# Performance work log

Hardware: AMD Instinct MI355X
Metric: run time of the kernel (lower is better)

Reference implementation:

```python
import jax, jax.numpy as jnp
import numpy as np

TOP_K = 2
EPS = 1e-8

def setup_inputs() -> dict:
    key = jax.random.key(0)
    k1, k2 = jax.random.split(key)
    T, D, E = 16384, 4096, 128  # tokens, d_model, num_experts
    x = jax.random.normal(k1, (T, D), dtype=jnp.float32)
    W = jax.random.normal(k2, (E, D), dtype=jnp.float32) * (1.0 / np.sqrt(D))
    b = jnp.zeros((E,), dtype=jnp.float32)
    return {"x": x, "W": W, "b": b}

def reference(x, W, b):
    # gate linear: [T, D] @ [D, E] -> [T, E]
    logits = jnp.einsum('td,ed->te', x, W) + b
    probs = jax.nn.softmax(logits, axis=-1)
    top_k_probs, top_k_indices = jax.lax.top_k(probs, TOP_K)
    top_k_probs = top_k_probs / (jnp.sum(top_k_probs, axis=-1, keepdims=True) + EPS)
    return (top_k_indices, top_k_probs)
```

## Files before the change

### kernel.cpp

```cpp
#include <hip/hip_runtime.h>
#include <math.h>


#define T_TOKENS 16384
#define D_K      4096
#define N_EXP    128
#define TOK_BLK  64
#define KSTEP    64
#define NITER    (D_K / KSTEP)

typedef float  f32x4  __attribute__((ext_vector_type(4)));
typedef short  bf16x8 __attribute__((ext_vector_type(8)));
typedef float  fragc  __attribute__((ext_vector_type(4)));

__device__ __forceinline__ unsigned short bf16_rne(float f) {
    unsigned u = __float_as_uint(f);
    u += 0x7FFFu + ((u >> 16) & 1u);
    return (unsigned short)(u >> 16);
}
__device__ __forceinline__ float bf16f(unsigned short h) {
    return __uint_as_float(((unsigned)h) << 16);
}

__device__ __forceinline__ int a_off(int G, int l) {
    const int L  = G * 64 + l;
    const int sw = ((L >> 3) ^ G) & 7;
    return (L << 4) ^ (sw << 4);
}

__global__ __launch_bounds__(256)
void prep_w(const float* __restrict__ W,
            short* __restrict__ wh, short* __restrict__ wl) {
    const int gid = blockIdx.x * 256 + threadIdx.x;
    const int l   = gid & 63;
    const int ntk = gid >> 6;
    const int e   = ((ntk & 7) << 4) + (l & 15);
    const int k   = ((ntk >> 3) << 5) + ((l >> 4) << 3);
    const float* src = W + (size_t)e * D_K + k;
    const f32x4 v0 = *(const f32x4*)src;
    const f32x4 v1 = *(const f32x4*)(src + 4);
    bf16x8 hv, lv;
#pragma unroll
    for (int j = 0; j < 8; ++j) {
        const float f = (j < 4) ? v0[j] : v1[j - 4];
        const unsigned short hh = bf16_rne(f);
        hv[j] = (short)hh;
        lv[j] = (short)bf16_rne(f - bf16f(hh));
    }
    *(bf16x8*)(wh + (size_t)gid * 8) = hv;
    *(bf16x8*)(wl + (size_t)gid * 8) = lv;
}

#define LOGSTRIDE 140
#define MERGE_OFF (64 * LOGSTRIDE * 4)
#define SMEM_SZ   (MERGE_OFF + 64 * 8 * 9 * 4)

__global__ __launch_bounds__(512, 2)
void router_mfma(const float* __restrict__ x,
                 const short* __restrict__ wh,
                 const short* __restrict__ wl,
                 const float* __restrict__ bvec,
                 float* __restrict__ out) {
    __shared__ __align__(16) char smem[SMEM_SZ];

    const int tid  = threadIdx.x;
    const int lane = tid & 63;
    const int w    = tid >> 6;
    const int wm   = w >> 2;
    const int wn   = w & 3;
    const int g    = blockIdx.x;

    const int s_tok = tid >> 3;
    const int s_kc8 = tid & 7;
    const float* xsrc = x + (size_t)(g * TOK_BLK + s_tok) * D_K + s_kc8 * 8;
    const int G_s   = ((s_kc8 >> 2) << 2) + (s_tok >> 4);
    const int l_s   = (s_tok & 15) | ((s_kc8 & 3) << 4);
    const int off_s = a_off(G_s, l_s);

    f32x4 ld0, ld1;
    auto issue = [&](int t) {
        const float* p = xsrc + (size_t)t * KSTEP;
        ld0 = *(const f32x4*)p;
        ld1 = *(const f32x4*)(p + 4);
    };
    auto commit = [&](int bufbase) {
        bf16x8 hv, lv;
#pragma unroll
        for (int j = 0; j < 8; ++j) {
            const float f = (j < 4) ? ld0[j] : ld1[j - 4];
            const unsigned short hh = bf16_rne(f);
            hv[j] = (short)hh;
            lv[j] = (short)bf16_rne(f - bf16f(hh));
        }
        *(bf16x8*)(smem + bufbase + off_s)        = hv;
        *(bf16x8*)(smem + bufbase + 8192 + off_s) = lv;
    };

    const short* base_h = wh + ((size_t)(wn * 2) * 64 + lane) * 8;
    const short* base_l = wl + ((size_t)(wn * 2) * 64 + lane) * 8;

    fragc acc[2][2];
#pragma unroll
    for (int mi = 0; mi < 2; ++mi)
#pragma unroll
        for (int nt = 0; nt < 2; ++nt)
            acc[mi][nt] = (fragc){0.f, 0.f, 0.f, 0.f};

    issue(0);
    commit(0);
    issue(1);
    __syncthreads();

    for (int t = 0; t < NITER; ++t) {
        const int cur = (t & 1) << 14;

        if (t + 1 < NITER) {
            commit(cur ^ (1 << 14));
            if (t + 2 < NITER) issue(t + 2);
        }

        bf16x8 bh[2][2], bl[2][2];
#pragma unroll
        for (int kb = 0; kb < 2; ++kb) {
            const size_t kofs = (size_t)(2 * t + kb) * 4096;
#pragma unroll
            for (int nt = 0; nt < 2; ++nt) {
                bh[kb][nt] = *(const bf16x8*)(base_h + kofs + nt * 512);
                bl[kb][nt] = *(const bf16x8*)(base_l + kofs + nt * 512);
            }
        }

#pragma unroll
        for (int kb = 0; kb < 2; ++kb) {
            bf16x8 ah[2], al[2];
#pragma unroll
            for (int mi = 0; mi < 2; ++mi) {
                const int off = a_off(kb * 4 + wm * 2 + mi, lane);
                ah[mi] = *(const bf16x8*)(smem + cur + off);
                al[mi] = *(const bf16x8*)(smem + cur + 8192 + off);
            }
#pragma unroll
            for (int mi = 0; mi < 2; ++mi)
#pragma unroll
                for (int nt = 0; nt < 2; ++nt) {
                    acc[mi][nt] = __builtin_amdgcn_mfma_f32_16x16x32_bf16(
                        ah[mi], bh[kb][nt], acc[mi][nt], 0, 0, 0);
                    acc[mi][nt] = __builtin_amdgcn_mfma_f32_16x16x32_bf16(
                        al[mi], bh[kb][nt], acc[mi][nt], 0, 0, 0);
                    acc[mi][nt] = __builtin_amdgcn_mfma_f32_16x16x32_bf16(
                        ah[mi], bl[kb][nt], acc[mi][nt], 0, 0, 0);
                }
        }
        __syncthreads();
    }

    float* lg = (float*)smem;
#pragma unroll
    for (int mi = 0; mi < 2; ++mi) {
        const int row0 = wm * 32 + mi * 16 + ((lane >> 4) << 2);
#pragma unroll
        for (int nt = 0; nt < 2; ++nt) {
            const int col = wn * 32 + nt * 16 + (lane & 15);
#pragma unroll
            for (int j = 0; j < 4; ++j)
                lg[(row0 + j) * LOGSTRIDE + col] = acc[mi][nt][j];
        }
    }
    __syncthreads();

    const int tok = tid & 63;
    const int q   = tid >> 6;
    const float* lrow = lg + tok * LOGSTRIDE + q * 16;
    const float* brow = bvec + q * 16;
    float v1 = -INFINITY, v2 = -INFINITY;
    int   i1 = 0, i2 = 0;
#pragma unroll
    for (int c = 0; c < 16; ++c) {
        const float lv = lrow[c] + brow[c];
        if (lv > v1)      { v2 = v1; i2 = i1; v1 = lv; i1 = c; }
        else if (lv > v2) { v2 = lv; i2 = c; }
    }
    float Z = 0.f;
#pragma unroll
    for (int c = 0; c < 16; ++c) Z += expf(lrow[c] + brow[c] - v1);

    float* mrow = (float*)(smem + MERGE_OFF) + (tok * 8 + q) * 9;
    mrow[0] = v1; mrow[1] = (float)(q * 16 + i1);
    mrow[2] = v2; mrow[3] = (float)(q * 16 + i2);
    mrow[4] = Z;
    __syncthreads();

    if (tid < 64) {
        const float* m0 = (float*)(smem + MERGE_OFF) + tid * 72;
        float V1 = m0[0], I1 = m0[1], V2 = m0[2], I2 = m0[3], Zs = m0[4];
#pragma unroll
        for (int q2 = 1; q2 < 8; ++q2) {
            const float* mq = m0 + q2 * 9;
            const float a1 = mq[0], ai1 = mq[1], a2 = mq[2], ai2 = mq[3], Zq = mq[4];
            const float M  = fmaxf(V1, a1);
            Zs = Zs * expf(V1 - M) + Zq * expf(a1 - M);
            if (a1 > V1)      { V2 = V1; I2 = I1; V1 = a1; I1 = ai1; }
            else if (a1 > V2) { V2 = a1; I2 = ai1; }
            if (a2 > V2)      { V2 = a2; I2 = ai2; }
        }
        const float p1 = 1.0f / Zs;
        const float p2 = expf(V2 - V1) / Zs;
        const float s  = p1 + p2 + 1e-8f;
        const int tokG = g * TOK_BLK + tid;
        float2* oidx  = (float2*)out;
        float2* oprob = ((float2*)out) + T_TOKENS;
        oidx[tokG]  = make_float2(I1, I2);
        oprob[tokG] = make_float2(p1 / s, p2 / s);
    }
}

extern "C" void kernel_launch(void* const* d_in, const int* in_sizes, int n_in,
                              void* d_out, int out_size, void* d_ws, size_t ws_size,
                              hipStream_t stream) {
    (void)in_sizes; (void)n_in; (void)out_size; (void)ws_size;
    const float* x = (const float*)d_in[0];
    const float* W = (const float*)d_in[1];
    const float* b = (const float*)d_in[2];
    float* out = (float*)d_out;
    short* wh = (short*)d_ws;
    short* wl = (short*)d_ws + (size_t)N_EXP * D_K;

    prep_w<<<dim3(256), dim3(256), 0, stream>>>(W, wh, wl);
    router_mfma<<<dim3(T_TOKENS / TOK_BLK), dim3(512), 0, stream>>>(x, wh, wl, b, out);
}
```

Measured before the change: 421.3 us.

## Load activations directly into registers and drop LDS staging and barriers

Each wave now loads its own x rows straight from global memory into registers, double-buffered two steps ahead. The bf16 hi/lo split is done in registers rather than written to LDS, which removes the per-iteration __syncthreads. The hi part is now a truncation instead of round-to-nearest, while the residual still carries the remainder. In exchange, each x element is loaded by the 4 waves that share the same wm rows, so global and L2 traffic for x goes up and register pressure rises.

```diff
diff --git a/kernel.cpp b/kernel.cpp
--- a/kernel.cpp
+++ b/kernel.cpp
@@ -6,8 +6,7 @@
 #define D_K      4096
 #define N_EXP    128
 #define TOK_BLK  64
-#define KSTEP    64
-#define NITER    (D_K / KSTEP)
+#define NITER    64
 
 typedef float  f32x4  __attribute__((ext_vector_type(4)));
 typedef short  bf16x8 __attribute__((ext_vector_type(8)));
@@ -20,12 +19,6 @@
 }
 __device__ __forceinline__ float bf16f(unsigned short h) {
     return __uint_as_float(((unsigned)h) << 16);
-}
-
-__device__ __forceinline__ int a_off(int G, int l) {
-    const int L  = G * 64 + l;
-    const int sw = ((L >> 3) ^ G) & 7;
-    return (L << 4) ^ (sw << 4);
 }
 
 __global__ __launch_bounds__(256)
@@ -70,31 +63,9 @@
     const int wn   = w & 3;
     const int g    = blockIdx.x;
 
-    const int s_tok = tid >> 3;
-    const int s_kc8 = tid & 7;
-    const float* xsrc = x + (size_t)(g * TOK_BLK + s_tok) * D_K + s_kc8 * 8;
-    const int G_s   = ((s_kc8 >> 2) << 2) + (s_tok >> 4);
-    const int l_s   = (s_tok & 15) | ((s_kc8 & 3) << 4);
-    const int off_s = a_off(G_s, l_s);
-
-    f32x4 ld0, ld1;
-    auto issue = [&](int t) {
-        const float* p = xsrc + (size_t)t * KSTEP;
-        ld0 = *(const f32x4*)p;
-        ld1 = *(const f32x4*)(p + 4);
-    };
-    auto commit = [&](int bufbase) {
-        bf16x8 hv, lv;
-#pragma unroll
-        for (int j = 0; j < 8; ++j) {
-            const float f = (j < 4) ? ld0[j] : ld1[j - 4];
-            const unsigned short hh = bf16_rne(f);
-            hv[j] = (short)hh;
-            lv[j] = (short)bf16_rne(f - bf16f(hh));
-        }
-        *(bf16x8*)(smem + bufbase + off_s)        = hv;
-        *(bf16x8*)(smem + bufbase + 8192 + off_s) = lv;
-    };
+    const float* arow0 = x + (size_t)(g * TOK_BLK + wm * 32 + (lane & 15)) * D_K
+                           + ((lane >> 4) << 3);
+    const float* arow1 = arow0 + (size_t)16 * D_K;
 
     const short* base_h = wh + ((size_t)(wn * 2) * 64 + lane) * 8;
     const short* base_l = wl + ((size_t)(wn * 2) * 64 + lane) * 8;
@@ -106,19 +77,22 @@
         for (int nt = 0; nt < 2; ++nt)
             acc[mi][nt] = (fragc){0.f, 0.f, 0.f, 0.f};
 
-    issue(0);
-    commit(0);
-    issue(1);
-    __syncthreads();
-
-    for (int t = 0; t < NITER; ++t) {
-        const int cur = (t & 1) << 14;
-
-        if (t + 1 < NITER) {
-            commit(cur ^ (1 << 14));
-            if (t + 2 < NITER) issue(t + 2);
-        }
-
+    f32x4 Aa[2][2][2], Ab[2][2][2];
+
+    auto loadA = [&](f32x4 (&A)[2][2][2], int t) {
+        const float* p0 = arow0 + (size_t)t * 64;
+        const float* p1 = arow1 + (size_t)t * 64;
+        A[0][0][0] = *(const f32x4*)(p0);
+        A[0][0][1] = *(const f32x4*)(p0 + 4);
+        A[0][1][0] = *(const f32x4*)(p0 + 32);
+        A[0][1][1] = *(const f32x4*)(p0 + 36);
+        A[1][0][0] = *(const f32x4*)(p1);
+        A[1][0][1] = *(const f32x4*)(p1 + 4);
+        A[1][1][0] = *(const f32x4*)(p1 + 32);
+        A[1][1][1] = *(const f32x4*)(p1 + 36);
+    };
+
+    auto step = [&](f32x4 (&A)[2][2][2], int t) {
         bf16x8 bh[2][2], bl[2][2];
 #pragma unroll
         for (int kb = 0; kb < 2; ++kb) {
@@ -129,29 +103,40 @@
                 bl[kb][nt] = *(const bf16x8*)(base_l + kofs + nt * 512);
             }
         }
-
-#pragma unroll
-        for (int kb = 0; kb < 2; ++kb) {
-            bf16x8 ah[2], al[2];
-#pragma unroll
-            for (int mi = 0; mi < 2; ++mi) {
-                const int off = a_off(kb * 4 + wm * 2 + mi, lane);
-                ah[mi] = *(const bf16x8*)(smem + cur + off);
-                al[mi] = *(const bf16x8*)(smem + cur + 8192 + off);
-            }
+        bf16x8 ah[2][2], al[2][2];
+#pragma unroll
+        for (int kb = 0; kb < 2; ++kb)
+#pragma unroll
+            for (int mi = 0; mi < 2; ++mi)
+#pragma unroll
+                for (int j = 0; j < 8; ++j) {
+                    const float f = (j < 4) ? A[mi][kb][0][j] : A[mi][kb][1][j - 4];
+                    const unsigned u  = __float_as_uint(f);
+                    const unsigned hu = u & 0xFFFF0000u;
+                    ah[kb][mi][j] = (short)(u >> 16);
+                    al[kb][mi][j] = (short)bf16_rne(f - __uint_as_float(hu));
+                }
+        if (t + 2 < NITER) loadA(A, t + 2);
+#pragma unroll
+        for (int kb = 0; kb < 2; ++kb)
 #pragma unroll
             for (int mi = 0; mi < 2; ++mi)
 #pragma unroll
                 for (int nt = 0; nt < 2; ++nt) {
                     acc[mi][nt] = __builtin_amdgcn_mfma_f32_16x16x32_bf16(
-                        ah[mi], bh[kb][nt], acc[mi][nt], 0, 0, 0);
+                        ah[kb][mi], bh[kb][nt], acc[mi][nt], 0, 0, 0);
                     acc[mi][nt] = __builtin_amdgcn_mfma_f32_16x16x32_bf16(
-                        al[mi], bh[kb][nt], acc[mi][nt], 0, 0, 0);
+                        al[kb][mi], bh[kb][nt], acc[mi][nt], 0, 0, 0);
                     acc[mi][nt] = __builtin_amdgcn_mfma_f32_16x16x32_bf16(
-                        ah[mi], bl[kb][nt], acc[mi][nt], 0, 0, 0);
+                        ah[kb][mi], bl[kb][nt], acc[mi][nt], 0, 0, 0);
                 }
-        }
-        __syncthreads();
+    };
+
+    loadA(Aa, 0);
+    loadA(Ab, 1);
+    for (int t = 0; t < NITER; t += 2) {
+        step(Aa, t);
+        step(Ab, t + 1);
     }
 
     float* lg = (float*)smem;
```

Result: slower. 457.3 us (+8.5%).

## Halve token tile to 32, give each wave one expert tile, raise occupancy

Applied to the files above, without the earlier changes.

Shrinks the per-block token tile from 64 to 32 so each of the 8 waves owns one 16-expert column tile and two 16-token row tiles. LDS per block drops and launch bounds request 4 blocks per CU instead of 2. The W fragment loads are issued before the x commit, and __syncthreads is replaced by an explicit lgkmcnt wait plus barrier. Each W fragment now feeds only 32 tokens instead of 64, so L2 traffic for W per token doubles in exchange for more blocks to hide latency.

```diff
diff --git a/kernel.cpp b/kernel.cpp
--- a/kernel.cpp
+++ b/kernel.cpp
@@ -5,13 +5,13 @@
 #define T_TOKENS 16384
 #define D_K      4096
 #define N_EXP    128
-#define TOK_BLK  64
-#define KSTEP    64
-#define NITER    (D_K / KSTEP)
+#define TOK_BLK  32
+#define NITER    64
 
 typedef float  f32x4  __attribute__((ext_vector_type(4)));
 typedef short  bf16x8 __attribute__((ext_vector_type(8)));
 typedef float  fragc  __attribute__((ext_vector_type(4)));
+typedef unsigned int u32;
 
 __device__ __forceinline__ unsigned short bf16_rne(float f) {
     unsigned u = __float_as_uint(f);
@@ -51,11 +51,11 @@
     *(bf16x8*)(wl + (size_t)gid * 8) = lv;
 }
 
-#define LOGSTRIDE 140
-#define MERGE_OFF (64 * LOGSTRIDE * 4)
-#define SMEM_SZ   (MERGE_OFF + 64 * 8 * 9 * 4)
-
-__global__ __launch_bounds__(512, 2)
+#define LOGSTRIDE 129
+#define MERGE_OFF (TOK_BLK * LOGSTRIDE * 4)
+#define SMEM_SZ   (MERGE_OFF + TOK_BLK * 8 * 9 * 4)
+
+__global__ __launch_bounds__(512, 4)
 void router_mfma(const float* __restrict__ x,
                  const short* __restrict__ wh,
                  const short* __restrict__ wl,
@@ -66,132 +66,137 @@
     const int tid  = threadIdx.x;
     const int lane = tid & 63;
     const int w    = tid >> 6;
-    const int wm   = w >> 2;
-    const int wn   = w & 3;
     const int g    = blockIdx.x;
 
-    const int s_tok = tid >> 3;
-    const int s_kc8 = tid & 7;
-    const float* xsrc = x + (size_t)(g * TOK_BLK + s_tok) * D_K + s_kc8 * 8;
-    const int G_s   = ((s_kc8 >> 2) << 2) + (s_tok >> 4);
-    const int l_s   = (s_tok & 15) | ((s_kc8 & 3) << 4);
-    const int off_s = a_off(G_s, l_s);
-
-    f32x4 ld0, ld1;
-    auto issue = [&](int t) {
-        const float* p = xsrc + (size_t)t * KSTEP;
-        ld0 = *(const f32x4*)p;
-        ld1 = *(const f32x4*)(p + 4);
+    const int s_tok = tid >> 4;
+    const int s_k4  = tid & 15;
+    const float* xsrc = x + (size_t)(g * TOK_BLK + s_tok) * D_K + s_k4 * 4;
+    const int kb_s  = s_k4 >> 3;
+    const int c_s   = s_k4 & 7;
+    const int mt_s  = s_tok >> 4;
+    const int l_s   = (s_tok & 15) | ((c_s >> 1) << 4);
+    const int off_s = a_off(kb_s * 2 + mt_s, l_s) + (c_s & 1) * 8;
+
+    f32x4 ld;
+    auto issue = [&](int t) { ld = *(const f32x4*)(xsrc + (size_t)t * 64); };
+    auto commit = [&](int bufbase) {
+        u32 h[2], lo[2];
+#pragma unroll
+        for (int p = 0; p < 2; ++p) {
+            u32 hw = 0, lw = 0;
+#pragma unroll
+            for (int j = 0; j < 2; ++j) {
+                const float f = ld[p * 2 + j];
+                const unsigned short hh = bf16_rne(f);
+                const unsigned short ll = bf16_rne(f - bf16f(hh));
+                hw |= (u32)hh << (16 * j);
+                lw |= (u32)ll << (16 * j);
+            }
+            h[p] = hw; lo[p] = lw;
+        }
+        *(uint2*)(smem + bufbase + off_s)        = make_uint2(h[0], h[1]);
+        *(uint2*)(smem + bufbase + 4096 + off_s) = make_uint2(lo[0], lo[1]);
     };
-    auto commit = [&](int bufbase) {
-        bf16x8 hv, lv;
-#pragma unroll
-        for (int j = 0; j < 8; ++j) {
-            const float f = (j < 4) ? ld0[j] : ld1[j - 4];
-            const unsigned short hh = bf16_rne(f);
-            hv[j] = (short)hh;
-            lv[j] = (short)bf16_rne(f - bf16f(hh));
-        }
-        *(bf16x8*)(smem + bufbase + off_s)        = hv;
-        *(bf16x8*)(smem + bufbase + 8192 + off_s) = lv;
-    };
-
-    const short* base_h = wh + ((size_t)(wn * 2) * 64 + lane) * 8;
-    const short* base_l = wl + ((size_t)(wn * 2) * 64 + lane) * 8;
-
-    fragc acc[2][2];
-#pragma unroll
-    for (int mi = 0; mi < 2; ++mi)
-#pragma unroll
-        for (int nt = 0; nt < 2; ++nt)
-            acc[mi][nt] = (fragc){0.f, 0.f, 0.f, 0.f};
+
+    const short* base_h = wh + ((size_t)w * 64 + lane) * 8;
+    const short* base_l = wl + ((size_t)w * 64 + lane) * 8;
+
+    fragc acc0 = (fragc){0.f, 0.f, 0.f, 0.f};
+    fragc acc1 = (fragc){0.f, 0.f, 0.f, 0.f};
 
     issue(0);
     commit(0);
     issue(1);
-    __syncthreads();
+    asm volatile("s_waitcnt lgkmcnt(0)\n\ts_barrier" ::: "memory");
 
     for (int t = 0; t < NITER; ++t) {
-        const int cur = (t & 1) << 14;
-
-        if (t + 1 < NITER) {
-            commit(cur ^ (1 << 14));
-            if (t + 2 < NITER) issue(t + 2);
-        }
-
-        bf16x8 bh[2][2], bl[2][2];
+        const int cur = (t & 1) << 13;
+
+        bf16x8 bh[2], bl[2];
 #pragma unroll
         for (int kb = 0; kb < 2; ++kb) {
             const size_t kofs = (size_t)(2 * t + kb) * 4096;
-#pragma unroll
-            for (int nt = 0; nt < 2; ++nt) {
-                bh[kb][nt] = *(const bf16x8*)(base_h + kofs + nt * 512);
-                bl[kb][nt] = *(const bf16x8*)(base_l + kofs + nt * 512);
+            bh[kb] = *(const bf16x8*)(base_h + kofs);
+            bl[kb] = *(const bf16x8*)(base_l + kofs);
+        }
+
+        if (t + 1 < NITER) {
+            commit(cur ^ 8192);
+            if (t + 2 < NITER) issue(t + 2);
+        }
+
+        bf16x8 ah[2][2], al[2][2];
+#pragma unroll
+        for (int kb = 0; kb < 2; ++kb)
+#pragma unroll
+            for (int mi = 0; mi < 2; ++mi) {
+                const int off = a_off(kb * 2 + mi, lane);
+                ah[kb][mi] = *(const bf16x8*)(smem + cur + off);
+                al[kb][mi] = *(const bf16x8*)(smem + cur + 4096 + off);
             }
-        }
 
 #pragma unroll
         for (int kb = 0; kb < 2; ++kb) {
-            bf16x8 ah[2], al[2];
-#pragma unroll
-            for (int mi = 0; mi < 2; ++mi) {
-                const int off = a_off(kb * 4 + wm * 2 + mi, lane);
-                ah[mi] = *(const bf16x8*)(smem + cur + off);
-                al[mi] = *(const bf16x8*)(smem + cur + 8192 + off);
+            acc0 = __builtin_amdgcn_mfma_f32_16x16x32_bf16(ah[kb][0], bh[kb], acc0, 0, 0, 0);
+            acc0 = __builtin_amdgcn_mfma_f32_16x16x32_bf16(al[kb][0], bh[kb], acc0, 0, 0, 0);
+            acc0 = __builtin_amdgcn_mfma_f32_16x16x32_bf16(ah[kb][0], bl[kb], acc0, 0, 0, 0);
+            acc1 = __builtin_amdgcn_mfma_f32_16x16x32_bf16(ah[kb][1], bh[kb], acc1, 0, 0, 0);
+            acc1 = __builtin_amdgcn_mfma_f32_16x16x32_bf16(al[kb][1], bh[kb], acc1, 0, 0, 0);
+            acc1 = __builtin_amdgcn_mfma_f32_16x16x32_bf16(ah[kb][1], bl[kb], acc1, 0, 0, 0);
+        }
+
+        asm volatile("s_waitcnt lgkmcnt(0)\n\ts_barrier" ::: "memory");
+    }
+    __syncthreads();
+
+    float* lg = (float*)smem;
+    {
+        const int col = w * 16 + (lane & 15);
+        const int r0  = (lane >> 4) << 2;
+#pragma unroll
+        for (int j = 0; j < 4; ++j) lg[(r0 + j) * LOGSTRIDE + col]      = acc0[j];
+#pragma unroll
+        for (int j = 0; j < 4; ++j) lg[(16 + r0 + j) * LOGSTRIDE + col] = acc1[j];
+    }
+    __syncthreads();
+
+    float* mg = (float*)(smem + MERGE_OFF);
+    if (tid < 256) {
+        const int tok = tid & 31;
+        const int q   = tid >> 5;
+        const float* lrow = lg + tok * LOGSTRIDE + q * 16;
+        f32x4 lv4[4], bv4[4];
+#pragma unroll
+        for (int i = 0; i < 4; ++i) lv4[i] = *(const f32x4*)(lrow + i * 4);
+#pragma unroll
+        for (int i = 0; i < 4; ++i) bv4[i] = *(const f32x4*)(bvec + q * 16 + i * 4);
+        float v1 = -INFINITY, v2 = -INFINITY;
+        int   i1 = 0, i2 = 0;
+#pragma unroll
+        for (int i = 0; i < 4; ++i)
+#pragma unroll
+            for (int j = 0; j < 4; ++j) {
+                const int   c  = i * 4 + j;
+                const float lv = lv4[i][j] + bv4[i][j];
+                if (lv > v1)      { v2 = v1; i2 = i1; v1 = lv; i1 = c; }
+                else if (lv > v2) { v2 = lv; i2 = c; }
             }
-#pragma unroll
-            for (int mi = 0; mi < 2; ++mi)
-#pragma unroll
-                for (int nt = 0; nt < 2; ++nt) {
-                    acc[mi][nt] = __builtin_amdgcn_mfma_f32_16x16x32_bf16(
-                        ah[mi], bh[kb][nt], acc[mi][nt], 0, 0, 0);
-                    acc[mi][nt] = __builtin_amdgcn_mfma_f32_16x16x32_bf16(
-                        al[mi], bh[kb][nt], acc[mi][nt], 0, 0, 0);
-                    acc[mi][nt] = __builtin_amdgcn_mfma_f32_16x16x32_bf16(
-                        ah[mi], bl[kb][nt], acc[mi][nt], 0, 0, 0);
-                }
-        }
-        __syncthreads();
-    }
-
-    float* lg = (float*)smem;
-#pragma unroll
-    for (int mi = 0; mi < 2; ++mi) {
-        const int row0 = wm * 32 + mi * 16 + ((lane >> 4) << 2);
-#pragma unroll
-        for (int nt = 0; nt < 2; ++nt) {
-            const int col = wn * 32 + nt * 16 + (lane & 15);
+        float Z = 0.f;
+#pragma unroll
+        for (int i = 0; i < 4; ++i)
 #pragma unroll
             for (int j = 0; j < 4; ++j)
-                lg[(row0 + j) * LOGSTRIDE + col] = acc[mi][nt][j];
-        }
+                Z += expf(lv4[i][j] + bv4[i][j] - v1);
+
+        float* mrow = mg + (tok * 8 + q) * 9;
+        mrow[0] = v1; mrow[1] = (float)(q * 16 + i1);
+        mrow[2] = v2; mrow[3] = (float)(q * 16 + i2);
+        mrow[4] = Z;
     }
     __syncthreads();
 
-    const int tok = tid & 63;
-    const int q   = tid >> 6;
-    const float* lrow = lg + tok * LOGSTRIDE + q * 16;
-    const float* brow = bvec + q * 16;
-    float v1 = -INFINITY, v2 = -INFINITY;
-    int   i1 = 0, i2 = 0;
-#pragma unroll
-    for (int c = 0; c < 16; ++c) {
-        const float lv = lrow[c] + brow[c];
-        if (lv > v1)      { v2 = v1; i2 = i1; v1 = lv; i1 = c; }
-        else if (lv > v2) { v2 = lv; i2 = c; }
-    }
-    float Z = 0.f;
-#pragma unroll
-    for (int c = 0; c < 16; ++c) Z += expf(lrow[c] + brow[c] - v1);
-
-    float* mrow = (float*)(smem + MERGE_OFF) + (tok * 8 + q) * 9;
-    mrow[0] = v1; mrow[1] = (float)(q * 16 + i1);
-    mrow[2] = v2; mrow[3] = (float)(q * 16 + i2);
-    mrow[4] = Z;
-    __syncthreads();
-
-    if (tid < 64) {
-        const float* m0 = (float*)(smem + MERGE_OFF) + tid * 72;
+    if (tid < TOK_BLK) {
+        const float* m0 = mg + tid * 72;
         float V1 = m0[0], I1 = m0[1], V2 = m0[2], I2 = m0[3], Zs = m0[4];
 #pragma unroll
         for (int q2 = 1; q2 < 8; ++q2) {
```

New measurement: 428.4 us. No clear change (+1.7%).
